# Kernel optimization log

Hardware: AMD Instinct MI355X
Metric: run time of the kernel (lower is better)

Reference implementation:

```python
import jax, jax.numpy as jnp
import numpy as np

N_NODES = 50000
N_EDGES = 400000
HID = 128
EPS_GEN = 1e-7  # GENConv message eps


def layernorm(x, w, b, eps=1e-5):
    mu = x.mean(-1, keepdims=True)
    var = x.var(-1, keepdims=True)
    return (x - mu) / jnp.sqrt(var + eps) * w + b


def segment_softmax(v, seg, n):
    # per-channel softmax over edges sharing the same destination node
    m = jax.ops.segment_max(v, seg, num_segments=n)
    e = jnp.exp(v - m[seg])
    s = jax.ops.segment_sum(e, seg, num_segments=n)
    return e / (s[seg] + 1e-16)


def genconv(x, src, dst, w1, b1, lnw, lnb, w2, b2, t):
    # GENConv(aggr='softmax', t learnable, mlp num_layers=2, norm='layer'), no edge_attr
    n = x.shape[0]
    msg = jax.nn.relu(x[src]) + EPS_GEN            # [E, H]
    alpha = segment_softmax(msg * t, dst, n)       # [E, H]
    aggr = jax.ops.segment_sum(msg * alpha, dst, num_segments=n)  # [N, H]
    h = x + aggr                                   # residual self term
    h = layernorm(h @ w1 + b1, lnw, lnb)           # Linear(H, 2H) + LayerNorm + ReLU
    return jax.nn.relu(h) @ w2 + b2                # Linear(2H, H)


def setup_inputs() -> dict:
    key = jax.random.key(0)
    ks = jax.random.split(key, 30)
    rn = lambda k, shape, s=0.02: jax.random.normal(k, shape, jnp.float32) * s
    inp = {}
    inp['x'] = jax.random.normal(ks[0], (N_NODES, 1024), jnp.float32)
    inp['edge_index'] = jax.random.randint(ks[1], (2, N_EDGES), 0, N_NODES, jnp.int64 if jax.config.jax_enable_x64 else jnp.int32)
    inp['fc_w'] = rn(ks[2], (1024, HID)); inp['fc_b'] = jnp.zeros((HID,), jnp.float32)
    inp['conv_w1'] = rn(ks[3], (3, HID, 2 * HID)); inp['conv_b1'] = jnp.zeros((3, 2 * HID), jnp.float32)
    inp['conv_lnw'] = jnp.ones((3, 2 * HID), jnp.float32); inp['conv_lnb'] = jnp.zeros((3, 2 * HID), jnp.float32)
    inp['conv_w2'] = rn(ks[4], (3, 2 * HID, HID)); inp['conv_b2'] = jnp.zeros((3, HID), jnp.float32)
    inp['conv_t'] = jnp.ones((3,), jnp.float32)
    inp['norm_w'] = jnp.ones((3, HID), jnp.float32); inp['norm_b'] = jnp.zeros((3, HID), jnp.float32)
    D = 4 * HID  # 512
    inp['phi_w'] = rn(ks[5], (D, D)); inp['phi_b'] = jnp.zeros((D,), jnp.float32)
    inp['attn_a_w'] = rn(ks[6], (D, D)); inp['attn_a_b'] = jnp.zeros((D,), jnp.float32)
    inp['attn_b_w'] = rn(ks[7], (D, D)); inp['attn_b_b'] = jnp.zeros((D,), jnp.float32)
    inp['attn_c_w'] = rn(ks[8], (D, 1)); inp['attn_c_b'] = jnp.zeros((1,), jnp.float32)
    inp['rho_w'] = rn(ks[9], (D, D)); inp['rho_b'] = jnp.zeros((D,), jnp.float32)
    inp['cls_w'] = rn(ks[10], (D, 4)); inp['cls_b'] = jnp.zeros((4,), jnp.float32)
    return inp


def reference(x, edge_index, fc_w, fc_b, conv_w1, conv_b1, conv_lnw, conv_lnb,
              conv_w2, conv_b2, conv_t, norm_w, norm_b, phi_w, phi_b,
              attn_a_w, attn_a_b, attn_b_w, attn_b_b, attn_c_w, attn_c_b,
              rho_w, rho_b, cls_w, cls_b):
    src, dst = edge_index[0], edge_index[1]
    # fc (dropout = identity in eval)
    x = jax.nn.relu(x @ fc_w + fc_b)               # [N, 128]
    x_ = x
    # layers[0].conv only (no norm/act/residual)
    x = genconv(x, src, dst, conv_w1[0], conv_b1[0], conv_lnw[0], conv_lnb[0],
                conv_w2[0], conv_b2[0], conv_t[0])
    x_ = jnp.concatenate([x_, x], axis=1)
    # DeepGCNLayer block='res': h = act(norm(conv(x))); x = x + h
    for i in (1, 2):
        h = genconv(x, src, dst, conv_w1[i], conv_b1[i], conv_lnw[i], conv_lnb[i],
                    conv_w2[i], conv_b2[i], conv_t[i])
        h = jax.nn.relu(layernorm(h, norm_w[i], norm_b[i]))
        x = x + h
        x_ = jnp.concatenate([x_, x], axis=1)
    h = jax.nn.relu(x_ @ phi_w + phi_b)            # path_phi, [N, 512]
    a = jnp.tanh(h @ attn_a_w + attn_a_b)
    b = jax.nn.sigmoid(h @ attn_b_w + attn_b_b)
    A = (a * b) @ attn_c_w + attn_c_b              # [N, 1]
    A = jax.nn.softmax(A.T, axis=1)                # [1, N]
    hp = A @ h                                     # [1, 512] attention pooling
    hp = jax.nn.relu(hp @ rho_w + rho_b)[0]        # squeeze -> [512]
    logits = (hp @ cls_w + cls_b)[None, :]         # [1, 4]
    return logits
```

## Files before the change

### kernel.cpp

```cpp
#include <hip/hip_runtime.h>
#include <hip/hip_bf16.h>
#include <math.h>

typedef __bf16 bf16_t;
typedef __attribute__((ext_vector_type(8))) __bf16 bf16x8;
typedef __attribute__((ext_vector_type(2))) __bf16 bf16x2;
typedef __attribute__((ext_vector_type(4))) float f32x4;

__device__ __forceinline__ void gld_lds16(const void* g, void* s) {
    __builtin_amdgcn_global_load_lds(
        (__attribute__((address_space(1))) unsigned int*)g,
        (__attribute__((address_space(3))) unsigned int*)s,
        16, 0, 0);
}

__device__ __forceinline__ int2 sw_decode(int orig, int nwg, int NT) {
    int q = nwg >> 3, r = nwg & 7, xcd = orig & 7, idx = orig >> 3;
    int wg = (xcd < r ? xcd * (q + 1) : r * (q + 1) + (xcd - r) * q) + idx;
    int bx = wg / NT, by = wg - bx * NT;
    return make_int2(bx, by);
}

__device__ __forceinline__ void tconv_tile(const float* __restrict__ in, bf16_t* __restrict__ out,
                                           int R, int C, int rs, int ro, int bx, int by)
{
    __shared__ float tile[32][33];
    int bc = bx * 32, br = by * 32;
    int tx = threadIdx.x & 31, ty = threadIdx.x >> 5;
    #pragma unroll
    for (int i = 0; i < 32; i += 8) {
        int r = br + ty + i, c = bc + tx;
        tile[ty + i][tx] = (r < R && c < C) ? in[(long)r * C + c] : 0.f;
    }
    __syncthreads();
    #pragma unroll
    for (int i = 0; i < 32; i += 8) {
        int c = bc + ty + i, r = br + tx;
        if (c < C && r < R) out[((long)c * rs + ro) * R + r] = (bf16_t)tile[tx][ty + i];
    }
}

__global__ __launch_bounds__(256) void k_prep(const float* __restrict__ fc_w, bf16_t* __restrict__ fcT,
                                              const float* __restrict__ conv_w1, bf16_t* __restrict__ w1T,
                                              const float* __restrict__ conv_w2, bf16_t* __restrict__ w2T,
                                              const float* __restrict__ phi_w, bf16_t* __restrict__ phiT,
                                              const float* __restrict__ aw, const float* __restrict__ bw,
                                              bf16_t* __restrict__ Bcat,
                                              const float* __restrict__ abias, const float* __restrict__ bbias,
                                              float* __restrict__ bias_cat)
{
    int b = blockIdx.x;
    if (b < 128) {
        tconv_tile(fc_w, fcT, 1024, 128, 1, 0, b & 3, b >> 2);
    } else if (b < 224) {
        int i = (b - 128) >> 5, bb = (b - 128) & 31;
        tconv_tile(conv_w1 + (size_t)i * 128 * 256, w1T + (size_t)i * 256 * 128, 128, 256, 1, 0, bb & 7, bb >> 3);
    } else if (b < 320) {
        int i = (b - 224) >> 5, bb = (b - 224) & 31;
        tconv_tile(conv_w2 + (size_t)i * 256 * 128, w2T + (size_t)i * 128 * 256, 256, 128, 1, 0, bb & 3, bb >> 2);
    } else if (b < 576) {
        int bb = b - 320;
        tconv_tile(phi_w, phiT, 512, 512, 1, 0, bb & 15, bb >> 4);
    } else if (b < 832) {
        int bb = b - 576;
        tconv_tile(aw, Bcat, 512, 512, 2, 0, bb & 15, bb >> 4);
    } else if (b < 1088) {
        int bb = b - 832;
        tconv_tile(bw, Bcat, 512, 512, 2, 1, bb & 15, bb >> 4);
    } else {
        int i = (b - 1088) * 256 + threadIdx.x;
        if (i < 512) { bias_cat[2 * i] = abias[i]; bias_cat[2 * i + 1] = bbias[i]; }
    }
}

__global__ __launch_bounds__(256) void k_deg(const int* __restrict__ dst, int* __restrict__ deg, int E)
{
    int e = blockIdx.x * 256 + threadIdx.x;
    if (e < E) atomicAdd(&deg[dst[e]], 1);
}

__global__ __launch_bounds__(1024) void k_scan_a(const int* __restrict__ deg, int* __restrict__ loc,
                                                 int* __restrict__ bsum, int n)
{
    __shared__ int wsum[16];
    int t = threadIdx.x, lane = t & 63, wid = t >> 6;
    int idx = blockIdx.x * 1024 + t;
    int v = (idx < n) ? deg[idx] : 0;
    int x = v;
    #pragma unroll
    for (int d = 1; d < 64; d <<= 1) { int o = __shfl_up(x, d); if (lane >= d) x += o; }
    if (lane == 63) wsum[wid] = x;
    __syncthreads();
    if (wid == 0 && lane < 16) {
        int y = wsum[lane];
        #pragma unroll
        for (int d = 1; d < 16; d <<= 1) { int o = __shfl_up(y, d); if (lane >= d) y += o; }
        wsum[lane] = y;
    }
    __syncthreads();
    int wbase = (wid == 0) ? 0 : wsum[wid - 1];
    if (idx < n) loc[idx] = wbase + x - v;
    if (t == 1023) bsum[blockIdx.x] = wsum[15];
}

__global__ __launch_bounds__(64) void k_scan_b(const int* __restrict__ bsum, int nb,
                                               int* __restrict__ boff, int* __restrict__ off_n)
{
    int lane = threadIdx.x;
    int base = 0;
    for (int c = 0; c < nb; c += 64) {
        int i = c + lane;
        int v = (i < nb) ? bsum[i] : 0;
        int x = v;
        #pragma unroll
        for (int d = 1; d < 64; d <<= 1) { int o = __shfl_up(x, d); if (lane >= d) x += o; }
        if (i < nb) boff[i] = base + x - v;
        base += __shfl(x, 63);
    }
    if (lane == 0) *off_n = base;
}

__global__ __launch_bounds__(1024) void k_scan_c(const int* __restrict__ loc, const int* __restrict__ boff,
                                                 int* __restrict__ off, int* __restrict__ cursor, int n)
{
    int idx = blockIdx.x * 1024 + threadIdx.x;
    if (idx < n) { int v = loc[idx] + boff[blockIdx.x]; off[idx] = v; cursor[idx] = v; }
}

__global__ __launch_bounds__(256) void k_fill(const int* __restrict__ src, const int* __restrict__ dst,
                                              int* __restrict__ cursor, int* __restrict__ csr, int E)
{
    int e = blockIdx.x * 256 + threadIdx.x;
    if (e < E) {
        int d = dst[e];
        int pos = atomicAdd(&cursor[d], 1);
        csr[pos] = src[e];
    }
}

__global__ __launch_bounds__(256) void k_agg(const bf16_t* __restrict__ X,
                                             const int* __restrict__ off, const int* __restrict__ csr,
                                             bf16_t* __restrict__ haux,
                                             const float* __restrict__ tptr, int ti, int Nn)
{
    int w = (blockIdx.x * 256 + threadIdx.x) >> 6;
    if (w >= Nn) return;
    int lane = threadIdx.x & 63;
    float t = tptr[ti];
    int e0 = off[w], e1 = off[w + 1];
    float m0 = -__builtin_inff(), m1 = -__builtin_inff();
    float s0 = 0.f, s1 = 0.f, g0 = 0.f, g1 = 0.f;

    auto proc = [&](bf16x2 xv) {
        float msg0 = fmaxf((float)xv[0], 0.f) + 1e-7f;
        float msg1 = fmaxf((float)xv[1], 0.f) + 1e-7f;
        float v0 = msg0 * t, v1 = msg1 * t;
        if (v0 > m0) { float sc = __expf(m0 - v0); s0 *= sc; g0 *= sc; m0 = v0; }
        float p0 = __expf(v0 - m0); s0 += p0; g0 += msg0 * p0;
        if (v1 > m1) { float sc = __expf(m1 - v1); s1 *= sc; g1 *= sc; m1 = v1; }
        float p1 = __expf(v1 - m1); s1 += p1; g1 += msg1 * p1;
    };

    int e = e0;
    for (; e + 4 <= e1; e += 4) {
        int ia = csr[e], ib = csr[e + 1], ic = csr[e + 2], id = csr[e + 3];
        bf16x2 va = *(const bf16x2*)(X + (long)ia * 128 + lane * 2);
        bf16x2 vb = *(const bf16x2*)(X + (long)ib * 128 + lane * 2);
        bf16x2 vc = *(const bf16x2*)(X + (long)ic * 128 + lane * 2);
        bf16x2 vd = *(const bf16x2*)(X + (long)id * 128 + lane * 2);
        proc(va); proc(vb); proc(vc); proc(vd);
    }
    for (; e < e1; e++) {
        int s = csr[e];
        bf16x2 xv = *(const bf16x2*)(X + (long)s * 128 + lane * 2);
        proc(xv);
    }
    float a0 = g0 / (s0 + 1e-16f);
    float a1 = g1 / (s1 + 1e-16f);
    bf16x2 xr = *(const bf16x2*)(X + (long)w * 128 + lane * 2);
    bf16_t* outp = haux + (long)w * 128 + lane * 2;
    outp[0] = (bf16_t)((float)xr[0] + a0);
    outp[1] = (bf16_t)((float)xr[1] + a1);
}

template<int BM, int EPI>
__global__ __launch_bounds__((BM == 256) ? 512 : 256, 4)
void k_gemm1(const bf16_t* __restrict__ A, int lda,
             const bf16_t* __restrict__ BT,
             const float* __restrict__ bias,
             bf16_t* __restrict__ Cout, int ldc,
             int M, int K, int NT,
             const float* __restrict__ cw,
             float* __restrict__ sout)
{
    constexpr int THREADS = (BM == 256) ? 512 : 256;
    constexpr int ACH = BM * 8 / THREADS;
    constexpr int BCH = 128 * 8 / THREADS;
    __shared__ __align__(16) bf16_t lA[BM * 64];
    __shared__ __align__(16) bf16_t lB[128 * 64];
    int2 bxy = sw_decode(blockIdx.x, gridDim.x, NT);
    const int m0 = bxy.x * BM, n0 = bxy.y * 128;
    const int tid = threadIdx.x, lane = tid & 63, wid = tid >> 6;
    const int rbase = (wid >> 1) * 64, cbase = (wid & 1) * 64;
    const int lrow = lane & 15, kg = lane >> 4;
    const int uw = tid & ~63;

    f32x4 acc[4][4];
    #pragma unroll
    for (int m = 0; m < 4; m++)
        #pragma unroll
        for (int n = 0; n < 4; n++)
            #pragma unroll
            for (int r = 0; r < 4; r++) acc[m][n][r] = 0.f;

    auto stage = [&](int k0) {
        #pragma unroll
        for (int c = 0; c < ACH; c++) {
            int s = c * THREADS + tid, row = s >> 3, k8s = (s & 7) ^ (row & 7);
            int gr = m0 + row; gr = gr < M ? gr : M - 1;
            gld_lds16(A + (long)gr * lda + k0 + k8s * 8, lA + (c * THREADS + uw) * 8);
        }
        #pragma unroll
        for (int c = 0; c < BCH; c++) {
            int s = c * THREADS + tid, row = s >> 3, k8s = (s & 7) ^ (row & 7);
            gld_lds16(BT + (long)(n0 + row) * K + k0 + k8s * 8, lB + (c * THREADS + uw) * 8);
        }
    };
    auto compute = [&]() {
        #pragma unroll
        for (int ks = 0; ks < 2; ks++) {
            int k8 = ks * 4 + kg;
            bf16x8 af[4], bfr[4];
            #pragma unroll
            for (int m = 0; m < 4; m++) {
                int r = rbase + m * 16 + lrow;
                af[m] = *(const bf16x8*)&lA[(r * 8 + (k8 ^ (r & 7))) * 8];
            }
            #pragma unroll
            for (int n = 0; n < 4; n++) {
                int r = cbase + n * 16 + lrow;
                bfr[n] = *(const bf16x8*)&lB[(r * 8 + (k8 ^ (r & 7))) * 8];
            }
            #pragma unroll
            for (int m = 0; m < 4; m++)
                #pragma unroll
                for (int n = 0; n < 4; n++)
                    acc[m][n] = __builtin_amdgcn_mfma_f32_16x16x32_bf16(af[m], bfr[n], acc[m][n], 0, 0, 0);
        }
    };

    for (int k0 = 0; k0 < K; k0 += 64) {
        stage(k0);
        __syncthreads();
        compute();
        __syncthreads();
    }

    if constexpr (EPI == 5) {
        #pragma unroll
        for (int m = 0; m < 4; m++) {
            #pragma unroll
            for (int r = 0; r < 4; r++) {
                int row = m0 + rbase + m * 16 + kg * 4 + r;
                float val = 0.f;
                #pragma unroll
                for (int n = 0; n < 4; n++) {
                    int col = n0 + cbase + n * 16 + lrow;
                    float xv = acc[m][n][r] + bias[col];
                    int odd = col & 1;
                    float z = odd ? xv : 2.f * xv;
                    float sg = 1.f / (1.f + __expf(-z));
                    float f = odd ? sg : (2.f * sg - 1.f);
                    float partner = __shfl_xor(f, 1);
                    float prod = f * partner;
                    val += odd ? 0.f : prod * cw[col >> 1];
                }
                #pragma unroll
                for (int o = 1; o < 16; o <<= 1) val += __shfl_xor(val, o);
                if (lrow == 0 && row < M) atomicAdd(&sout[row], val);
            }
        }
    } else {
        #pragma unroll
        for (int m = 0; m < 4; m++) {
            #pragma unroll
            for (int r = 0; r < 4; r++) {
                int row = m0 + rbase + m * 16 + kg * 4 + r;
                if (row >= M) continue;
                #pragma unroll
                for (int n = 0; n < 4; n++) {
                    int col = n0 + cbase + n * 16 + lrow;
                    float xv = fmaxf(acc[m][n][r] + bias[col], 0.f);
                    Cout[(long)row * ldc + col] = (bf16_t)xv;
                }
            }
        }
    }
}

__global__ __launch_bounds__(256) void k_gemm_fc(const float* __restrict__ Aptr, int lda,
                                                 const bf16_t* __restrict__ BT,
                                                 const float* __restrict__ bias,
                                                 bf16_t* __restrict__ Cout, int ldc,
                                                 bf16_t* __restrict__ Cout2,
                                                 int M, int K)
{
    constexpr int BUFA = 64 * 64;
    constexpr int BUFB = 128 * 64;
    __shared__ __align__(16) bf16_t lA[2 * BUFA];
    __shared__ __align__(16) bf16_t lB[2 * BUFB];
    const int m0 = blockIdx.x * 64, n0 = 0;
    const int tid = threadIdx.x, lane = tid & 63, wid = tid >> 6;
    const int rbase = wid * 16;
    const int lrow = lane & 15, kg = lane >> 4;
    const int ub = tid & 192;

    f32x4 acc[8];
    #pragma unroll
    for (int n = 0; n < 8; n++)
        #pragma unroll
        for (int r = 0; r < 4; r++) acc[n][r] = 0.f;

    f32x4 fa[4];

    auto stageB = [&](int k0, int buf) {
        #pragma unroll
        for (int c = 0; c < 4; c++) {
            int s = c * 256 + tid, row = s >> 3, k8s = (s & 7) ^ (row & 7);
            gld_lds16(BT + (long)(n0 + row) * K + k0 + k8s * 8, lB + buf * BUFB + (c * 256 + ub) * 8);
        }
    };
    auto loadA_f32 = [&](int k0) {
        #pragma unroll
        for (int c = 0; c < 2; c++) {
            int s = c * 256 + tid, row = s >> 3, k8s = (s & 7) ^ (row & 7);
            int grow = m0 + row;
            if (grow < M) {
                const float* sp = Aptr + (long)grow * lda + k0 + k8s * 8;
                fa[2 * c] = *(const f32x4*)sp;
                fa[2 * c + 1] = *(const f32x4*)(sp + 4);
            } else {
                #pragma unroll
                for (int j = 0; j < 4; j++) { fa[2 * c][j] = 0.f; fa[2 * c + 1][j] = 0.f; }
            }
        }
    };
    auto writeA = [&](int buf) {
        #pragma unroll
        for (int c = 0; c < 2; c++) {
            int s = c * 256 + tid;
            bf16x8 v;
            #pragma unroll
            for (int j = 0; j < 4; j++) { v[j] = (bf16_t)fa[2 * c][j]; v[4 + j] = (bf16_t)fa[2 * c + 1][j]; }
            *(bf16x8*)&lA[buf * BUFA + s * 8] = v;
        }
    };
    auto compute = [&](int buf) {
        #pragma unroll
        for (int ks = 0; ks < 2; ks++) {
            int k8 = ks * 4 + kg;
            int ra = rbase + lrow;
            bf16x8 af = *(const bf16x8*)&lA[buf * BUFA + (ra * 8 + (k8 ^ (ra & 7))) * 8];
            #pragma unroll
            for (int n = 0; n < 8; n++) {
                int r = n * 16 + lrow;
                bf16x8 bf = *(const bf16x8*)&lB[buf * BUFB + (r * 8 + (k8 ^ (r & 7))) * 8];
                acc[n] = __builtin_amdgcn_mfma_f32_16x16x32_bf16(af, bf, acc[n], 0, 0, 0);
            }
        }
    };

    const int nt = K >> 6;
    loadA_f32(0); writeA(0);
    stageB(0, 0);
    __syncthreads();
    int cur = 0;
    for (int t = 0; t < nt - 1; t++) {
        int nk = (t + 1) << 6;
        loadA_f32(nk);
        stageB(nk, cur ^ 1);
        compute(cur);
        __syncthreads();
        writeA(cur ^ 1);
        __syncthreads();
        cur ^= 1;
    }
    compute(cur);

    #pragma unroll
    for (int r = 0; r < 4; r++) {
        int row = m0 + rbase + kg * 4 + r;
        if (row >= M) continue;
        #pragma unroll
        for (int n = 0; n < 8; n++) {
            int col = n * 16 + lrow;
            float xv = fmaxf(acc[n][r] + bias[col], 0.f);
            Cout[(long)row * ldc + col] = (bf16_t)xv;
            Cout2[(long)row * 128 + col] = (bf16_t)xv;
        }
    }
}

template<int MODE>
__global__ __launch_bounds__(256) void k_convf(const bf16_t* __restrict__ A,
                                               const bf16_t* __restrict__ B1T,
                                               const float* __restrict__ b1,
                                               const float* __restrict__ lnw, const float* __restrict__ lnb,
                                               const bf16_t* __restrict__ B2T,
                                               const float* __restrict__ b2,
                                               const float* __restrict__ nw, const float* __restrict__ nb,
                                               const float* __restrict__ xs_in,
                                               bf16_t* __restrict__ xcat_out,
                                               float* __restrict__ xs_out, bf16_t* __restrict__ xl_out,
                                               int M)
{
    __shared__ __align__(16) bf16_t lA[64 * 128];
    __shared__ __align__(16) bf16_t lB1[256 * 128];
    __shared__ __align__(16) bf16_t h1b[64 * 256];
    __shared__ __align__(16) bf16_t lB2a[128 * 128];
    bf16_t* lB2b = lB1;

    const int m0 = blockIdx.x * 64;
    const int tid = threadIdx.x, lane = tid & 63, w = tid >> 6;
    const int lrow = lane & 15, kg = lane >> 4;
    const int ub = tid & 192;

    #pragma unroll
    for (int c = 0; c < 4; c++) {
        int s = c * 256 + tid, row = s >> 4, sl = s & 15;
        int k8 = (sl & 8) | ((sl & 7) ^ (row & 7));
        int gr = m0 + row; gr = gr < M ? gr : M - 1;
        gld_lds16(A + (long)gr * 128 + k8 * 8, lA + (c * 256 + ub) * 8);
    }
    #pragma unroll
    for (int c = 0; c < 16; c++) {
        int s = c * 256 + tid, row = s >> 4, sl = s & 15;
        int k8 = (sl & 8) | ((sl & 7) ^ (row & 7));
        gld_lds16(B1T + (long)row * 128 + k8 * 8, lB1 + (c * 256 + ub) * 8);
    }
    #pragma unroll
    for (int c = 0; c < 8; c++) {
        int s = c * 256 + tid, row = s >> 4, sl = s & 15;
        int k8 = (sl & 8) | ((sl & 7) ^ (row & 7));
        gld_lds16(B2T + (long)row * 256 + k8 * 8, lB2a + (c * 256 + ub) * 8);
    }
    asm volatile("s_waitcnt vmcnt(8)" ::: "memory");
    __builtin_amdgcn_s_barrier();

    f32x4 acc1[16];
    #pragma unroll
    for (int n = 0; n < 16; n++)
        #pragma unroll
        for (int r = 0; r < 4; r++) acc1[n][r] = 0.f;
    #pragma unroll
    for (int ks = 0; ks < 4; ks++) {
        int k8 = ks * 4 + kg;
        int ra = w * 16 + lrow;
        bf16x8 af = *(const bf16x8*)&lA[(ra * 16 + ((k8 & 8) | ((k8 & 7) ^ (ra & 7)))) * 8];
        #pragma unroll
        for (int n = 0; n < 16; n++) {
            int rb = n * 16 + lrow;
            bf16x8 bf = *(const bf16x8*)&lB1[(rb * 16 + ((k8 & 8) | ((k8 & 7) ^ (rb & 7)))) * 8];
            acc1[n] = __builtin_amdgcn_mfma_f32_16x16x32_bf16(af, bf, acc1[n], 0, 0, 0);
        }
    }

    #pragma unroll
    for (int r = 0; r < 4; r++) {
        int row = w * 16 + kg * 4 + r;
        float xv[16], s1 = 0.f, s2 = 0.f;
        #pragma unroll
        for (int n = 0; n < 16; n++) {
            int col = n * 16 + lrow;
            xv[n] = acc1[n][r] + b1[col];
            s1 += xv[n]; s2 += xv[n] * xv[n];
        }
        #pragma unroll
        for (int o = 1; o < 16; o <<= 1) { s1 += __shfl_xor(s1, o); s2 += __shfl_xor(s2, o); }
        float mu = s1 * (1.f / 256.f);
        float var = s2 * (1.f / 256.f) - mu * mu;
        float rstd = rsqrtf(var + 1e-5f);
        #pragma unroll
        for (int n = 0; n < 16; n++) {
            int col = n * 16 + lrow;
            float y = fmaxf((xv[n] - mu) * rstd * lnw[col] + lnb[col], 0.f);
            int chunk = (col >> 3);
            int cs = (chunk & 24) | ((chunk & 7) ^ (row & 7));
            h1b[row * 256 + cs * 8 + (col & 7)] = (bf16_t)y;
        }
    }

    asm volatile("s_waitcnt vmcnt(0)" ::: "memory");
    __builtin_amdgcn_s_barrier();

    #pragma unroll
    for (int c = 0; c < 8; c++) {
        int s = c * 256 + tid, row = s >> 4, sl = s & 15;
        int k8l = (sl & 8) | ((sl & 7) ^ (row & 7));
        gld_lds16(B2T + (long)row * 256 + (16 + k8l) * 8, lB2b + (c * 256 + ub) * 8);
    }

    f32x4 acc2[8];
    #pragma unroll
    for (int n = 0; n < 8; n++)
        #pragma unroll
        for (int r = 0; r < 4; r++) acc2[n][r] = 0.f;
    #pragma unroll
    for (int ks = 0; ks < 4; ks++) {
        int k8 = ks * 4 + kg;
        int ra = w * 16 + lrow;
        bf16x8 af = *(const bf16x8*)&h1b[(ra * 32 + ((k8 & 24) | ((k8 & 7) ^ (ra & 7)))) * 8];
        #pragma unroll
        for (int n = 0; n < 8; n++) {
            int rb = n * 16 + lrow;
            bf16x8 bf = *(const bf16x8*)&lB2a[(rb * 16 + ((k8 & 8) | ((k8 & 7) ^ (rb & 7)))) * 8];
            acc2[n] = __builtin_amdgcn_mfma_f32_16x16x32_bf16(af, bf, acc2[n], 0, 0, 0);
        }
    }
    asm volatile("s_waitcnt vmcnt(0)" ::: "memory");
    __builtin_amdgcn_s_barrier();
    #pragma unroll
    for (int ks = 0; ks < 4; ks++) {
        int k8 = 16 + ks * 4 + kg;
        int k8l = k8 - 16;
        int ra = w * 16 + lrow;
        bf16x8 af = *(const bf16x8*)&h1b[(ra * 32 + ((k8 & 24) | ((k8 & 7) ^ (ra & 7)))) * 8];
        #pragma unroll
        for (int n = 0; n < 8; n++) {
            int rb = n * 16 + lrow;
            bf16x8 bf = *(const bf16x8*)&lB2b[(rb * 16 + ((k8l & 8) | ((k8l & 7) ^ (rb & 7)))) * 8];
            acc2[n] = __builtin_amdgcn_mfma_f32_16x16x32_bf16(af, bf, acc2[n], 0, 0, 0);
        }
    }

    #pragma unroll
    for (int r = 0; r < 4; r++) {
        int row = m0 + w * 16 + kg * 4 + r;
        float xv[8];
        #pragma unroll
        for (int n = 0; n < 8; n++) xv[n] = acc2[n][r] + b2[n * 16 + lrow];
        if constexpr (MODE == 1) {
            float s1 = 0.f, s2 = 0.f;
            #pragma unroll
            for (int n = 0; n < 8; n++) { s1 += xv[n]; s2 += xv[n] * xv[n]; }
            #pragma unroll
            for (int o = 1; o < 16; o <<= 1) { s1 += __shfl_xor(s1, o); s2 += __shfl_xor(s2, o); }
            float mu = s1 * (1.f / 128.f);
            float var = s2 * (1.f / 128.f) - mu * mu;
            float rstd = rsqrtf(var + 1e-5f);
            if (row < M) {
                #pragma unroll
                for (int n = 0; n < 8; n++) {
                    int col = n * 16 + lrow;
                    xv[n] = xs_in[(long)row * 128 + col] + fmaxf((xv[n] - mu) * rstd * nw[col] + nb[col], 0.f);
                }
            }
        }
        if (row < M) {
            #pragma unroll
            for (int n = 0; n < 8; n++) {
                int col = n * 16 + lrow;
                xcat_out[(long)row * 512 + col] = (bf16_t)xv[n];
                if (xs_out) xs_out[(long)row * 128 + col] = xv[n];
                if (xl_out) xl_out[(long)row * 128 + col] = (bf16_t)xv[n];
            }
        }
    }
}

__global__ __launch_bounds__(256) void k_sred_a(const float* __restrict__ sN, int Nn,
                                                float* __restrict__ pmax, float* __restrict__ psum)
{
    __shared__ float red[4];
    int t = threadIdx.x, lane = t & 63, wid = t >> 6;
    int stride = gridDim.x * 256;
    float m = -__builtin_inff();
    for (int i = blockIdx.x * 256 + t; i < Nn; i += stride) m = fmaxf(m, sN[i]);
    #pragma unroll
    for (int o = 32; o >= 1; o >>= 1) m = fmaxf(m, __shfl_xor(m, o));
    if (lane == 0) red[wid] = m;
    __syncthreads();
    float bm = fmaxf(fmaxf(red[0], red[1]), fmaxf(red[2], red[3]));
    float s = 0.f;
    for (int i = blockIdx.x * 256 + t; i < Nn; i += stride) s += __expf(sN[i] - bm);
    #pragma unroll
    for (int o = 32; o >= 1; o >>= 1) s += __shfl_xor(s, o);
    __syncthreads();
    if (lane == 0) red[wid] = s;
    __syncthreads();
    if (t == 0) {
        pmax[blockIdx.x] = bm;
        psum[blockIdx.x] = red[0] + red[1] + red[2] + red[3];
    }
}

__global__ __launch_bounds__(64) void k_sred_b(const float* __restrict__ pmax, const float* __restrict__ psum,
                                               int nb, float* __restrict__ red)
{
    int lane = threadIdx.x;
    float m = (lane < nb) ? pmax[lane] : -__builtin_inff();
    #pragma unroll
    for (int o = 32; o >= 1; o >>= 1) m = fmaxf(m, __shfl_xor(m, o));
    float s = (lane < nb) ? psum[lane] * __expf(pmax[lane] - m) : 0.f;
    #pragma unroll
    for (int o = 32; o >= 1; o >>= 1) s += __shfl_xor(s, o);
    if (lane == 0) { red[0] = m; red[1] = s; }
}

__global__ __launch_bounds__(256) void k_pool(const bf16_t* __restrict__ h, const float* __restrict__ sN,
                                              const float* __restrict__ red, float* __restrict__ hp, int Nn)
{
    __shared__ float part[4][512];
    int t = threadIdx.x, lane = t & 63, w = t >> 6;
    float m = red[0], inv = 1.f / red[1];
    float acc[8];
    #pragma unroll
    for (int j = 0; j < 8; j++) acc[j] = 0.f;
    for (int n = blockIdx.x * 4 + w; n < Nn; n += gridDim.x * 4) {
        float wgt = __expf(sN[n] - m) * inv;
        bf16x8 v = *(const bf16x8*)(h + (long)n * 512 + lane * 8);
        #pragma unroll
        for (int j = 0; j < 8; j++) acc[j] += wgt * (float)v[j];
    }
    #pragma unroll
    for (int j = 0; j < 8; j++) part[w][lane * 8 + j] = acc[j];
    __syncthreads();
    #pragma unroll
    for (int c = 0; c < 2; c++) {
        int col = c * 256 + t;
        float s = part[0][col] + part[1][col] + part[2][col] + part[3][col];
        atomicAdd(&hp[col], s);
    }
}

__global__ __launch_bounds__(256) void k_tail_a(const float* __restrict__ hp,
                                                const float* __restrict__ rho_w, const float* __restrict__ rho_b,
                                                float* __restrict__ h2g)
{
    __shared__ float hs[512];
    __shared__ float part[256];
    int t = threadIdx.x;
    hs[t] = hp[t]; hs[t + 256] = hp[t + 256];
    __syncthreads();
    int col = blockIdx.x * 64 + (t & 63);
    int ks = t >> 6;
    float acc = 0.f;
    for (int k = ks * 128; k < ks * 128 + 128; k++) acc += hs[k] * rho_w[(long)k * 512 + col];
    part[t] = acc;
    __syncthreads();
    if (ks == 0) {
        float v = part[t] + part[t + 64] + part[t + 128] + part[t + 192] + rho_b[col];
        h2g[col] = fmaxf(v, 0.f);
    }
}

__global__ __launch_bounds__(256) void k_tail_b(const float* __restrict__ h2g,
                                                const float* __restrict__ cls_w, const float* __restrict__ cls_b,
                                                float* __restrict__ out)
{
    __shared__ float wred[4][4];
    int t = threadIdx.x, lane = t & 63, wid = t >> 6;
    float a0 = 0.f, a1 = 0.f, a2 = 0.f, a3 = 0.f;
    for (int d = t; d < 512; d += 256) {
        float h = h2g[d];
        a0 += h * cls_w[d * 4 + 0];
        a1 += h * cls_w[d * 4 + 1];
        a2 += h * cls_w[d * 4 + 2];
        a3 += h * cls_w[d * 4 + 3];
    }
    #pragma unroll
    for (int o = 32; o >= 1; o >>= 1) {
        a0 += __shfl_xor(a0, o); a1 += __shfl_xor(a1, o);
        a2 += __shfl_xor(a2, o); a3 += __shfl_xor(a3, o);
    }
    if (lane == 0) { wred[wid][0] = a0; wred[wid][1] = a1; wred[wid][2] = a2; wred[wid][3] = a3; }
    __syncthreads();
    if (t < 4)
        out[t] = cls_b[t] + wred[0][t] + wred[1][t] + wred[2][t] + wred[3][t];
}

extern "C" void kernel_launch(void* const* d_in, const int* in_sizes, int n_in,
                              void* d_out, int out_size, void* d_ws, size_t ws_size,
                              hipStream_t stream)
{
    const float* x       = (const float*)d_in[0];
    const int*   eidx    = (const int*)  d_in[1];
    const float* fc_w    = (const float*)d_in[2];
    const float* fc_b    = (const float*)d_in[3];
    const float* conv_w1 = (const float*)d_in[4];
    const float* conv_b1 = (const float*)d_in[5];
    const float* conv_lnw= (const float*)d_in[6];
    const float* conv_lnb= (const float*)d_in[7];
    const float* conv_w2 = (const float*)d_in[8];
    const float* conv_b2 = (const float*)d_in[9];
    const float* conv_t  = (const float*)d_in[10];
    const float* norm_w  = (const float*)d_in[11];
    const float* norm_b  = (const float*)d_in[12];
    const float* phi_w   = (const float*)d_in[13];
    const float* phi_b   = (const float*)d_in[14];
    const float* aw      = (const float*)d_in[15];
    const float* ab      = (const float*)d_in[16];
    const float* bw      = (const float*)d_in[17];
    const float* bb      = (const float*)d_in[18];
    const float* cwp     = (const float*)d_in[19];
    const float* rho_w   = (const float*)d_in[21];
    const float* rho_b   = (const float*)d_in[22];
    const float* cls_w   = (const float*)d_in[23];
    const float* cls_b   = (const float*)d_in[24];

    const int Nn = in_sizes[0] / 1024;
    const int E  = in_sizes[1] / 2;

    char* p = (char*)d_ws;
    auto carve = [&](size_t bytes) { char* r = p; p += (bytes + 255) & ~(size_t)255; return r; };

    bf16_t* x_cat_b = (bf16_t*)carve((size_t)Nn * 512 * 2);
    bf16_t* haux    = (bf16_t*)carve((size_t)Nn * 128 * 2);
    float*  xs1     = (float*)carve((size_t)Nn * 128 * 4);
    float*  xs2     = (float*)carve((size_t)Nn * 128 * 4);
    bf16_t* xl0     = (bf16_t*)carve((size_t)Nn * 128 * 2);
    bf16_t* xl1     = (bf16_t*)carve((size_t)Nn * 128 * 2);
    bf16_t* xl2     = (bf16_t*)carve((size_t)Nn * 128 * 2);
    bf16_t* h_phi   = (bf16_t*)carve((size_t)Nn * 512 * 2);
    bf16_t* fcT  = (bf16_t*)carve((size_t)128 * 1024 * 2);
    bf16_t* w1T  = (bf16_t*)carve((size_t)3 * 256 * 128 * 2);
    bf16_t* w2T  = (bf16_t*)carve((size_t)3 * 128 * 256 * 2);
    bf16_t* phiT = (bf16_t*)carve((size_t)512 * 512 * 2);
    bf16_t* Bcat = (bf16_t*)carve((size_t)1024 * 512 * 2);
    float* bias_cat = (float*)carve(1024 * 4);
    int*   deg    = (int*)carve((size_t)Nn * 4);
    int*   loc    = (int*)carve((size_t)Nn * 4);
    int*   bsum   = (int*)carve(256 * 4);
    int*   boff   = (int*)carve(256 * 4);
    int*   offArr = (int*)carve((size_t)(Nn + 1) * 4);
    int*   cursor = (int*)carve((size_t)Nn * 4);
    int*   csr    = (int*)carve((size_t)E * 4);
    float* sN     = (float*)carve((size_t)Nn * 4);
    float* pmax   = (float*)carve(64 * 4);
    float* psum   = (float*)carve(64 * 4);
    float* red    = (float*)carve(64);
    float* hp     = (float*)carve(512 * 4);
    float* h2g    = (float*)carve(512 * 4);

    hipMemsetAsync(deg, 0, (size_t)Nn * 4, stream);
    hipMemsetAsync(sN, 0, (size_t)Nn * 4, stream);
    hipMemsetAsync(hp, 0, 512 * 4, stream);

    k_prep<<<1090, 256, 0, stream>>>(fc_w, fcT, conv_w1, w1T, conv_w2, w2T, phi_w, phiT,
                                     aw, bw, Bcat, ab, bb, bias_cat);

    const int SB = (Nn + 1023) / 1024;
    k_deg<<<(E + 255) / 256, 256, 0, stream>>>(eidx + E, deg, E);
    k_scan_a<<<SB, 1024, 0, stream>>>(deg, loc, bsum, Nn);
    k_scan_b<<<1, 64, 0, stream>>>(bsum, SB, boff, offArr + Nn);
    k_scan_c<<<SB, 1024, 0, stream>>>(loc, boff, offArr, cursor, Nn);
    k_fill<<<(E + 255) / 256, 256, 0, stream>>>(eidx, eidx + E, cursor, csr, E);

    const int MT64  = (Nn + 63) / 64;
    const int MT256 = (Nn + 255) / 256;
    const int agB = (Nn + 3) / 4;

    k_gemm_fc<<<MT64, 256, 0, stream>>>(x, 1024, fcT, fc_b, x_cat_b, 512, xl0, Nn, 1024);

    const bf16_t* xls[3] = {xl0, xl1, xl2};
    for (int i = 0; i < 3; i++) {
        k_agg<<<agB, 256, 0, stream>>>(xls[i], offArr, csr, haux, conv_t, i, Nn);
        if (i == 0)
            k_convf<0><<<MT64, 256, 0, stream>>>(haux, w1T, conv_b1, conv_lnw, conv_lnb,
                                                 w2T, conv_b2, nullptr, nullptr, nullptr,
                                                 x_cat_b + 128, xs1, xl1, Nn);
        else if (i == 1)
            k_convf<1><<<MT64, 256, 0, stream>>>(haux, w1T + (size_t)256 * 128, conv_b1 + 256,
                                                 conv_lnw + 256, conv_lnb + 256,
                                                 w2T + (size_t)128 * 256, conv_b2 + 128,
                                                 norm_w + 128, norm_b + 128, xs1,
                                                 x_cat_b + 256, xs2, xl2, Nn);
        else
            k_convf<1><<<MT64, 256, 0, stream>>>(haux, w1T + (size_t)2 * 256 * 128, conv_b1 + 512,
                                                 conv_lnw + 512, conv_lnb + 512,
                                                 w2T + (size_t)2 * 128 * 256, conv_b2 + 256,
                                                 norm_w + 256, norm_b + 256, xs2,
                                                 x_cat_b + 384, nullptr, nullptr, Nn);
    }

    k_gemm1<256, 3><<<MT256 * 4, 512, 0, stream>>>(x_cat_b, 512, phiT, phi_b, h_phi, 512,
                                                   Nn, 512, 4, nullptr, nullptr);
    k_gemm1<256, 5><<<MT256 * 8, 512, 0, stream>>>(h_phi, 512, Bcat, bias_cat, nullptr, 0,
                                                   Nn, 512, 8, cwp, sN);
    k_sred_a<<<64, 256, 0, stream>>>(sN, Nn, pmax, psum);
    k_sred_b<<<1, 64, 0, stream>>>(pmax, psum, 64, red);
    k_pool<<<256, 256, 0, stream>>>(h_phi, sN, red, hp, Nn);
    k_tail_a<<<8, 256, 0, stream>>>(hp, rho_w, rho_b, h2g);
    k_tail_b<<<1, 256, 0, stream>>>(h2g, cls_w, cls_b, (float*)d_out);
}
```

Before: 632.4 us.

## Retile fc GEMM and conv fusion kernel, deepen aggregation gather unroll

The fc GEMM becomes a 128x128 tile with a 2x2 wave layout and 4x4 MFMA register blocks. It drops double buffering for a single-buffered loop with two barriers per step, and converts A to bf16 into a swizzled LDS layout. The fused conv kernel moves to 128-row tiles with 512 threads and aliases the hidden buffer onto the B1 LDS region and the second W2 half onto the A region, which reduces LDS use but adds a barrier. The aggregation gather loop is unrolled to 8 edges to raise memory-level parallelism. The larger tiles are meant to improve weight reuse, at the cost of fewer blocks and lost load/compute overlap in the fc GEMM.

```diff
diff --git a/kernel.cpp b/kernel.cpp
--- a/kernel.cpp
+++ b/kernel.cpp
@@ -162,13 +162,26 @@
     };
 
     int e = e0;
+    for (; e + 8 <= e1; e += 8) {
+        int i0 = csr[e],     i1 = csr[e + 1], i2 = csr[e + 2], i3 = csr[e + 3];
+        int i4 = csr[e + 4], i5 = csr[e + 5], i6 = csr[e + 6], i7 = csr[e + 7];
+        bf16x2 v0 = *(const bf16x2*)(X + (long)i0 * 128 + lane * 2);
+        bf16x2 v1 = *(const bf16x2*)(X + (long)i1 * 128 + lane * 2);
+        bf16x2 v2 = *(const bf16x2*)(X + (long)i2 * 128 + lane * 2);
+        bf16x2 v3 = *(const bf16x2*)(X + (long)i3 * 128 + lane * 2);
+        bf16x2 v4 = *(const bf16x2*)(X + (long)i4 * 128 + lane * 2);
+        bf16x2 v5 = *(const bf16x2*)(X + (long)i5 * 128 + lane * 2);
+        bf16x2 v6 = *(const bf16x2*)(X + (long)i6 * 128 + lane * 2);
+        bf16x2 v7 = *(const bf16x2*)(X + (long)i7 * 128 + lane * 2);
+        proc(v0); proc(v1); proc(v2); proc(v3); proc(v4); proc(v5); proc(v6); proc(v7);
+    }
     for (; e + 4 <= e1; e += 4) {
-        int ia = csr[e], ib = csr[e + 1], ic = csr[e + 2], id = csr[e + 3];
-        bf16x2 va = *(const bf16x2*)(X + (long)ia * 128 + lane * 2);
-        bf16x2 vb = *(const bf16x2*)(X + (long)ib * 128 + lane * 2);
-        bf16x2 vc = *(const bf16x2*)(X + (long)ic * 128 + lane * 2);
-        bf16x2 vd = *(const bf16x2*)(X + (long)id * 128 + lane * 2);
-        proc(va); proc(vb); proc(vc); proc(vd);
+        int i0 = csr[e], i1 = csr[e + 1], i2 = csr[e + 2], i3 = csr[e + 3];
+        bf16x2 v0 = *(const bf16x2*)(X + (long)i0 * 128 + lane * 2);
+        bf16x2 v1 = *(const bf16x2*)(X + (long)i1 * 128 + lane * 2);
+        bf16x2 v2 = *(const bf16x2*)(X + (long)i2 * 128 + lane * 2);
+        bf16x2 v3 = *(const bf16x2*)(X + (long)i3 * 128 + lane * 2);
+        proc(v0); proc(v1); proc(v2); proc(v3);
     }
     for (; e < e1; e++) {
         int s = csr[e];
@@ -298,111 +311,96 @@
     }
 }
 
-__global__ __launch_bounds__(256) void k_gemm_fc(const float* __restrict__ Aptr, int lda,
-                                                 const bf16_t* __restrict__ BT,
-                                                 const float* __restrict__ bias,
-                                                 bf16_t* __restrict__ Cout, int ldc,
-                                                 bf16_t* __restrict__ Cout2,
-                                                 int M, int K)
-{
-    constexpr int BUFA = 64 * 64;
-    constexpr int BUFB = 128 * 64;
-    __shared__ __align__(16) bf16_t lA[2 * BUFA];
-    __shared__ __align__(16) bf16_t lB[2 * BUFB];
-    const int m0 = blockIdx.x * 64, n0 = 0;
+__global__ __launch_bounds__(256) void k_gemm_fcP(const float* __restrict__ Aptr, int lda,
+                                                  const bf16_t* __restrict__ BT,
+                                                  const float* __restrict__ bias,
+                                                  bf16_t* __restrict__ Cout, int ldc,
+                                                  bf16_t* __restrict__ Cout2,
+                                                  int M, int K)
+{
+    __shared__ __align__(16) bf16_t lA[128 * 64];
+    __shared__ __align__(16) bf16_t lB[128 * 64];
+    const int m0 = blockIdx.x * 128;
     const int tid = threadIdx.x, lane = tid & 63, wid = tid >> 6;
-    const int rbase = wid * 16;
+    const int rbase = (wid >> 1) * 64, cbase = (wid & 1) * 64;
     const int lrow = lane & 15, kg = lane >> 4;
-    const int ub = tid & 192;
-
-    f32x4 acc[8];
-    #pragma unroll
-    for (int n = 0; n < 8; n++)
-        #pragma unroll
-        for (int r = 0; r < 4; r++) acc[n][r] = 0.f;
-
-    f32x4 fa[4];
-
-    auto stageB = [&](int k0, int buf) {
+    const int uw = tid & ~63;
+
+    f32x4 acc[4][4];
+    #pragma unroll
+    for (int m = 0; m < 4; m++)
+        #pragma unroll
+        for (int n = 0; n < 4; n++)
+            #pragma unroll
+            for (int r = 0; r < 4; r++) acc[m][n][r] = 0.f;
+
+    f32x4 fa[8];
+
+    for (int k0 = 0; k0 < K; k0 += 64) {
+        #pragma unroll
+        for (int c = 0; c < 4; c++) {
+            int s = c * 256 + tid, row = s >> 3, k8 = s & 7;
+            int gr = m0 + row; gr = gr < M ? gr : M - 1;
+            const float* sp = Aptr + (long)gr * lda + k0 + k8 * 8;
+            fa[2 * c] = *(const f32x4*)sp;
+            fa[2 * c + 1] = *(const f32x4*)(sp + 4);
+        }
         #pragma unroll
         for (int c = 0; c < 4; c++) {
             int s = c * 256 + tid, row = s >> 3, k8s = (s & 7) ^ (row & 7);
-            gld_lds16(BT + (long)(n0 + row) * K + k0 + k8s * 8, lB + buf * BUFB + (c * 256 + ub) * 8);
-        }
-    };
-    auto loadA_f32 = [&](int k0) {
-        #pragma unroll
-        for (int c = 0; c < 2; c++) {
-            int s = c * 256 + tid, row = s >> 3, k8s = (s & 7) ^ (row & 7);
-            int grow = m0 + row;
-            if (grow < M) {
-                const float* sp = Aptr + (long)grow * lda + k0 + k8s * 8;
-                fa[2 * c] = *(const f32x4*)sp;
-                fa[2 * c + 1] = *(const f32x4*)(sp + 4);
-            } else {
-                #pragma unroll
-                for (int j = 0; j < 4; j++) { fa[2 * c][j] = 0.f; fa[2 * c + 1][j] = 0.f; }
-            }
-        }
-    };
-    auto writeA = [&](int buf) {
-        #pragma unroll
-        for (int c = 0; c < 2; c++) {
-            int s = c * 256 + tid;
+            gld_lds16(BT + (long)row * K + k0 + k8s * 8, lB + (c * 256 + uw) * 8);
+        }
+        #pragma unroll
+        for (int c = 0; c < 4; c++) {
+            int s = c * 256 + tid, row = s >> 3, k8 = s & 7;
             bf16x8 v;
             #pragma unroll
             for (int j = 0; j < 4; j++) { v[j] = (bf16_t)fa[2 * c][j]; v[4 + j] = (bf16_t)fa[2 * c + 1][j]; }
-            *(bf16x8*)&lA[buf * BUFA + s * 8] = v;
-        }
-    };
-    auto compute = [&](int buf) {
+            *(bf16x8*)&lA[(row * 8 + (k8 ^ (row & 7))) * 8] = v;
+        }
+        __syncthreads();
         #pragma unroll
         for (int ks = 0; ks < 2; ks++) {
             int k8 = ks * 4 + kg;
-            int ra = rbase + lrow;
-            bf16x8 af = *(const bf16x8*)&lA[buf * BUFA + (ra * 8 + (k8 ^ (ra & 7))) * 8];
-            #pragma unroll
-            for (int n = 0; n < 8; n++) {
-                int r = n * 16 + lrow;
-                bf16x8 bf = *(const bf16x8*)&lB[buf * BUFB + (r * 8 + (k8 ^ (r & 7))) * 8];
-                acc[n] = __builtin_amdgcn_mfma_f32_16x16x32_bf16(af, bf, acc[n], 0, 0, 0);
+            bf16x8 af[4], bfr[4];
+            #pragma unroll
+            for (int m = 0; m < 4; m++) {
+                int r = rbase + m * 16 + lrow;
+                af[m] = *(const bf16x8*)&lA[(r * 8 + (k8 ^ (r & 7))) * 8];
             }
-        }
-    };
-
-    const int nt = K >> 6;
-    loadA_f32(0); writeA(0);
-    stageB(0, 0);
-    __syncthreads();
-    int cur = 0;
-    for (int t = 0; t < nt - 1; t++) {
-        int nk = (t + 1) << 6;
-        loadA_f32(nk);
-        stageB(nk, cur ^ 1);
-        compute(cur);
+            #pragma unroll
+            for (int n = 0; n < 4; n++) {
+                int r = cbase + n * 16 + lrow;
+                bfr[n] = *(const bf16x8*)&lB[(r * 8 + (k8 ^ (r & 7))) * 8];
+            }
+            #pragma unroll
+            for (int m = 0; m < 4; m++)
+                #pragma unroll
+                for (int n = 0; n < 4; n++)
+                    acc[m][n] = __builtin_amdgcn_mfma_f32_16x16x32_bf16(af[m], bfr[n], acc[m][n], 0, 0, 0);
+        }
         __syncthreads();
-        writeA(cur ^ 1);
-        __syncthreads();
-        cur ^= 1;
-    }
-    compute(cur);
-
-    #pragma unroll
-    for (int r = 0; r < 4; r++) {
-        int row = m0 + rbase + kg * 4 + r;
-        if (row >= M) continue;
-        #pragma unroll
-        for (int n = 0; n < 8; n++) {
-            int col = n * 16 + lrow;
-            float xv = fmaxf(acc[n][r] + bias[col], 0.f);
-            Cout[(long)row * ldc + col] = (bf16_t)xv;
-            Cout2[(long)row * 128 + col] = (bf16_t)xv;
+    }
+
+    #pragma unroll
+    for (int m = 0; m < 4; m++) {
+        #pragma unroll
+        for (int r = 0; r < 4; r++) {
+            int row = m0 + rbase + m * 16 + kg * 4 + r;
+            if (row >= M) continue;
+            #pragma unroll
+            for (int n = 0; n < 4; n++) {
+                int col = cbase + n * 16 + lrow;
+                float xv = fmaxf(acc[m][n][r] + bias[col], 0.f);
+                Cout[(long)row * ldc + col] = (bf16_t)xv;
+                Cout2[(long)row * 128 + col] = (bf16_t)xv;
+            }
         }
     }
 }
 
 template<int MODE>
-__global__ __launch_bounds__(256) void k_convf(const bf16_t* __restrict__ A,
+__global__ __launch_bounds__(512) void k_convf(const bf16_t* __restrict__ A,
                                                const bf16_t* __restrict__ B1T,
                                                const float* __restrict__ b1,
                                                const float* __restrict__ lnw, const float* __restrict__ lnb,
@@ -414,37 +412,37 @@
                                                float* __restrict__ xs_out, bf16_t* __restrict__ xl_out,
                                                int M)
 {
-    __shared__ __align__(16) bf16_t lA[64 * 128];
+    __shared__ __align__(16) bf16_t lA[128 * 128];
     __shared__ __align__(16) bf16_t lB1[256 * 128];
-    __shared__ __align__(16) bf16_t h1b[64 * 256];
     __shared__ __align__(16) bf16_t lB2a[128 * 128];
-    bf16_t* lB2b = lB1;
-
-    const int m0 = blockIdx.x * 64;
+    bf16_t* h1 = lB1;
+    bf16_t* lB2b = lA;
+
+    const int m0 = blockIdx.x * 128;
     const int tid = threadIdx.x, lane = tid & 63, w = tid >> 6;
     const int lrow = lane & 15, kg = lane >> 4;
-    const int ub = tid & 192;
+    const int uw = tid & ~63;
 
     #pragma unroll
     for (int c = 0; c < 4; c++) {
-        int s = c * 256 + tid, row = s >> 4, sl = s & 15;
+        int s = c * 512 + tid, row = s >> 4, sl = s & 15;
         int k8 = (sl & 8) | ((sl & 7) ^ (row & 7));
         int gr = m0 + row; gr = gr < M ? gr : M - 1;
-        gld_lds16(A + (long)gr * 128 + k8 * 8, lA + (c * 256 + ub) * 8);
-    }
-    #pragma unroll
-    for (int c = 0; c < 16; c++) {
-        int s = c * 256 + tid, row = s >> 4, sl = s & 15;
+        gld_lds16(A + (long)gr * 128 + k8 * 8, lA + (c * 512 + uw) * 8);
+    }
+    #pragma unroll
+    for (int c = 0; c < 8; c++) {
+        int s = c * 512 + tid, row = s >> 4, sl = s & 15;
         int k8 = (sl & 8) | ((sl & 7) ^ (row & 7));
-        gld_lds16(B1T + (long)row * 128 + k8 * 8, lB1 + (c * 256 + ub) * 8);
-    }
-    #pragma unroll
-    for (int c = 0; c < 8; c++) {
-        int s = c * 256 + tid, row = s >> 4, sl = s & 15;
+        gld_lds16(B1T + (long)row * 128 + k8 * 8, lB1 + (c * 512 + uw) * 8);
+    }
+    #pragma unroll
+    for (int c = 0; c < 4; c++) {
+        int s = c * 512 + tid, row = s >> 4, sl = s & 15;
         int k8 = (sl & 8) | ((sl & 7) ^ (row & 7));
-        gld_lds16(B2T + (long)row * 256 + k8 * 8, lB2a + (c * 256 + ub) * 8);
-    }
-    asm volatile("s_waitcnt vmcnt(8)" ::: "memory");
+        gld_lds16(B2T + (long)row * 256 + k8 * 8, lB2a + (c * 512 + uw) * 8);
+    }
+    asm volatile("s_waitcnt vmcnt(4)" ::: "memory");
     __builtin_amdgcn_s_barrier();
 
     f32x4 acc1[16];
@@ -465,15 +463,16 @@
         }
     }
 
+    float hv[4][16];
     #pragma unroll
     for (int r = 0; r < 4; r++) {
-        int row = w * 16 + kg * 4 + r;
-        float xv[16], s1 = 0.f, s2 = 0.f;
+        float s1 = 0.f, s2 = 0.f;
         #pragma unroll
         for (int n = 0; n < 16; n++) {
             int col = n * 16 + lrow;
-            xv[n] = acc1[n][r] + b1[col];
-            s1 += xv[n]; s2 += xv[n] * xv[n];
+            float xv = acc1[n][r] + b1[col];
+            hv[r][n] = xv;
+            s1 += xv; s2 += xv * xv;
         }
         #pragma unroll
         for (int o = 1; o < 16; o <<= 1) { s1 += __shfl_xor(s1, o); s2 += __shfl_xor(s2, o); }
@@ -483,21 +482,28 @@
         #pragma unroll
         for (int n = 0; n < 16; n++) {
             int col = n * 16 + lrow;
-            float y = fmaxf((xv[n] - mu) * rstd * lnw[col] + lnb[col], 0.f);
-            int chunk = (col >> 3);
+            hv[r][n] = fmaxf((hv[r][n] - mu) * rstd * lnw[col] + lnb[col], 0.f);
+        }
+    }
+
+    __builtin_amdgcn_s_barrier();
+
+    #pragma unroll
+    for (int r = 0; r < 4; r++) {
+        int row = w * 16 + kg * 4 + r;
+        #pragma unroll
+        for (int n = 0; n < 16; n++) {
+            int col = n * 16 + lrow;
+            int chunk = col >> 3;
             int cs = (chunk & 24) | ((chunk & 7) ^ (row & 7));
-            h1b[row * 256 + cs * 8 + (col & 7)] = (bf16_t)y;
-        }
-    }
-
-    asm volatile("s_waitcnt vmcnt(0)" ::: "memory");
-    __builtin_amdgcn_s_barrier();
-
-    #pragma unroll
-    for (int c = 0; c < 8; c++) {
-        int s = c * 256 + tid, row = s >> 4, sl = s & 15;
+            h1[row * 256 + cs * 8 + (col & 7)] = (bf16_t)hv[r][n];
+        }
+    }
+    #pragma unroll
+    for (int c = 0; c < 4; c++) {
+        int s = c * 512 + tid, row = s >> 4, sl = s & 15;
         int k8l = (sl & 8) | ((sl & 7) ^ (row & 7));
-        gld_lds16(B2T + (long)row * 256 + (16 + k8l) * 8, lB2b + (c * 256 + ub) * 8);
+        gld_lds16(B2T + (long)row * 256 + (16 + k8l) * 8, lB2b + (c * 512 + uw) * 8);
     }
 
     f32x4 acc2[8];
@@ -509,7 +515,7 @@
     for (int ks = 0; ks < 4; ks++) {
         int k8 = ks * 4 + kg;
         int ra = w * 16 + lrow;
-        bf16x8 af = *(const bf16x8*)&h1b[(ra * 32 + ((k8 & 24) | ((k8 & 7) ^ (ra & 7)))) * 8];
+        bf16x8 af = *(const bf16x8*)&h1[(ra * 32 + ((k8 & 24) | ((k8 & 7) ^ (ra & 7)))) * 8];
         #pragma unroll
         for (int n = 0; n < 8; n++) {
             int rb = n * 16 + lrow;
@@ -519,12 +525,13 @@
     }
     asm volatile("s_waitcnt vmcnt(0)" ::: "memory");
     __builtin_amdgcn_s_barrier();
+
     #pragma unroll
     for (int ks = 0; ks < 4; ks++) {
         int k8 = 16 + ks * 4 + kg;
         int k8l = k8 - 16;
         int ra = w * 16 + lrow;
-        bf16x8 af = *(const bf16x8*)&h1b[(ra * 32 + ((k8 & 24) | ((k8 & 7) ^ (ra & 7)))) * 8];
+        bf16x8 af = *(const bf16x8*)&h1[(ra * 32 + ((k8 & 24) | ((k8 & 7) ^ (ra & 7)))) * 8];
         #pragma unroll
         for (int n = 0; n < 8; n++) {
             int rb = n * 16 + lrow;
@@ -756,31 +763,31 @@
     k_scan_c<<<SB, 1024, 0, stream>>>(loc, boff, offArr, cursor, Nn);
     k_fill<<<(E + 255) / 256, 256, 0, stream>>>(eidx, eidx + E, cursor, csr, E);
 
-    const int MT64  = (Nn + 63) / 64;
+    const int MT128 = (Nn + 127) / 128;
     const int MT256 = (Nn + 255) / 256;
     const int agB = (Nn + 3) / 4;
 
-    k_gemm_fc<<<MT64, 256, 0, stream>>>(x, 1024, fcT, fc_b, x_cat_b, 512, xl0, Nn, 1024);
+    k_gemm_fcP<<<MT128, 256, 0, stream>>>(x, 1024, fcT, fc_b, x_cat_b, 512, xl0, Nn, 1024);
 
     const bf16_t* xls[3] = {xl0, xl1, xl2};
     for (int i = 0; i < 3; i++) {
         k_agg<<<agB, 256, 0, stream>>>(xls[i], offArr, csr, haux, conv_t, i, Nn);
         if (i == 0)
-            k_convf<0><<<MT64, 256, 0, stream>>>(haux, w1T, conv_b1, conv_lnw, conv_lnb,
-                                                 w2T, conv_b2, nullptr, nullptr, nullptr,
-                                                 x_cat_b + 128, xs1, xl1, Nn);
+            k_convf<0><<<MT128, 512, 0, stream>>>(haux, w1T, conv_b1, conv_lnw, conv_lnb,
+                                                  w2T, conv_b2, nullptr, nullptr, nullptr,
+                                                  x_cat_b + 128, xs1, xl1, Nn);
         else if (i == 1)
-            k_convf<1><<<MT64, 256, 0, stream>>>(haux, w1T + (size_t)256 * 128, conv_b1 + 256,
-                                                 conv_lnw + 256, conv_lnb + 256,
-                                                 w2T + (size_t)128 * 256, conv_b2 + 128,
-                                                 norm_w + 128, norm_b + 128, xs1,
-                                                 x_cat_b + 256, xs2, xl2, Nn);
+            k_convf<1><<<MT128, 512, 0, stream>>>(haux, w1T + (size_t)256 * 128, conv_b1 + 256,
+                                                  conv_lnw + 256, conv_lnb + 256,
+                                                  w2T + (size_t)128 * 256, conv_b2 + 128,
+                                                  norm_w + 128, norm_b + 128, xs1,
+                                                  x_cat_b + 256, xs2, xl2, Nn);
         else
-            k_convf<1><<<MT64, 256, 0, stream>>>(haux, w1T + (size_t)2 * 256 * 128, conv_b1 + 512,
-                                                 conv_lnw + 512, conv_lnb + 512,
-                                                 w2T + (size_t)2 * 128 * 256, conv_b2 + 256,
-                                                 norm_w + 256, norm_b + 256, xs2,
-                                                 x_cat_b + 384, nullptr, nullptr, Nn);
+            k_convf<1><<<MT128, 512, 0, stream>>>(haux, w1T + (size_t)2 * 256 * 128, conv_b1 + 512,
+                                                  conv_lnw + 512, conv_lnb + 512,
+                                                  w2T + (size_t)2 * 128 * 256, conv_b2 + 256,
+                                                  norm_w + 256, norm_b + 256, xs2,
+                                                  x_cat_b + 384, nullptr, nullptr, Nn);
     }
 
     k_gemm1<256, 3><<<MT256 * 4, 512, 0, stream>>>(x_cat_b, 512, phiT, phi_b, h_phi, 512,
```

Result: faster. 577.5 us (-8.7%).
